# Performance work log

Hardware: AMD Instinct MI355X
Metric: run time of the kernel (lower is better)

Reference implementation:

```python
import jax, jax.numpy as jnp
import numpy as np

N_NODES = 50000
N_EDGES = 800000
F_IN = 128
HIDDEN = 128
N_CLASSES = 40


def setup_inputs() -> dict:
    key = jax.random.key(0)
    ks = jax.random.split(key, 8)
    x = jax.random.normal(ks[0], (N_NODES, F_IN), dtype=jnp.float32)
    edge_index = jax.random.randint(ks[1], (2, N_EDGES), 0, N_NODES, dtype=jnp.int32)
    s_in = 1.0 / np.sqrt(F_IN)
    s_h = 1.0 / np.sqrt(HIDDEN)
    W1_l = jax.random.normal(ks[2], (F_IN, HIDDEN), jnp.float32) * s_in
    W1_r = jax.random.normal(ks[3], (F_IN, HIDDEN), jnp.float32) * s_in
    b1 = jnp.zeros((HIDDEN,), jnp.float32)
    W2_l = jax.random.normal(ks[4], (HIDDEN, N_CLASSES), jnp.float32) * s_h
    W2_r = jax.random.normal(ks[5], (HIDDEN, N_CLASSES), jnp.float32) * s_h
    b2 = jnp.zeros((N_CLASSES,), jnp.float32)
    return {"x": x, "edge_index": edge_index, "W1_l": W1_l, "W1_r": W1_r,
            "b1": b1, "W2_l": W2_l, "W2_r": W2_r, "b2": b2}


def _sage_conv(x, src, dst, W_l, W_r, b):
    # mean-aggregate neighbor features at dst, then linear transform + root weight
    msg = x[src]                                                  # [E, d] gather
    agg = jax.ops.segment_sum(msg, dst, num_segments=N_NODES)     # [N, d] scatter-add
    deg = jax.ops.segment_sum(jnp.ones((src.shape[0],), x.dtype), dst,
                              num_segments=N_NODES)
    agg = agg / jnp.maximum(deg, 1.0)[:, None]                    # mean aggregation
    return agg @ W_l + x @ W_r + b


def reference(x, edge_index, W1_l, W1_r, b1, W2_l, W2_r, b2):
    src, dst = edge_index[0], edge_index[1]
    h = jax.nn.relu(_sage_conv(x, src, dst, W1_l, W1_r, b1))
    # F.dropout(p=0.5, training=self.training) -> identity in eval mode
    out = jax.nn.relu(_sage_conv(h, src, dst, W2_l, W2_r, b2))
    return jax.nn.log_softmax(out, axis=-1)
```

## Files before the change

kernel.cpp:

```cpp
#include <hip/hip_runtime.h>

#define N_NODES 50000
#define N_EDGES 800000
#define F_IN 128
#define HIDDEN 128
#define N_CLASSES 40

#define NBUCKET 391
#define BUCKET_CAP 4096
#define BINA_CHUNK 2048
#define BINA_NBLK 391
#define PREP_ITEMS (N_NODES * 32 + 128 * 256 + 80 * 128)
#define PREP_NBLK (PREP_ITEMS / 256)

#define OFF_RS     0
#define OFF_BCNT   50004
#define OFF_INVDEG 100004
#define OFF_SRCS   150004
#define OFF_AB     950004
#define OFF_BINS   7350004
#define OFF_PB     7350004
#define OFF_Q      8350004
#define OFF_WT1    10550004
#define OFF_WT2    10566388

typedef short bf16x8 __attribute__((ext_vector_type(8)));
typedef float f32x4 __attribute__((ext_vector_type(4)));
typedef unsigned short u16x8 __attribute__((ext_vector_type(8)));

static __device__ __forceinline__ unsigned short f2bf(float f) {
  unsigned int u = __builtin_bit_cast(unsigned int, f);
  u = (u + 0x7fffu + ((u >> 16) & 1u)) >> 16;
  return (unsigned short)u;
}
static __device__ __forceinline__ float bf2f(unsigned short s) {
  unsigned int u = ((unsigned int)s) << 16;
  return __builtin_bit_cast(float, u);
}

__global__ __launch_bounds__(256) void k_binA_prep(
    const int* __restrict__ src, const int* __restrict__ dst,
    int* __restrict__ bcnt, int* __restrict__ bins,
    const float* __restrict__ x, const float* __restrict__ W1l,
    const float* __restrict__ W1r, const float* __restrict__ W2l,
    const float* __restrict__ W2r, unsigned short* __restrict__ Ab,
    unsigned short* __restrict__ Wt1, unsigned short* __restrict__ Wt2) {
  if (blockIdx.x >= BINA_NBLK) {
    int idx = (blockIdx.x - BINA_NBLK) * 256 + threadIdx.x;
    if (idx < N_NODES * 32) {
      int row = idx >> 5, c4 = (idx & 31) << 2;
      const float4 v = *(const float4*)(x + (size_t)row * F_IN + c4);
      ushort4 o;
      o.x = f2bf(v.x); o.y = f2bf(v.y); o.z = f2bf(v.z); o.w = f2bf(v.w);
      *(ushort4*)(Ab + (size_t)row * 256 + 128 + c4) = o;
      return;
    }
    idx -= N_NODES * 32;
    if (idx < 128 * 256) {
      int n = idx >> 8, k = idx & 255;
      float v = (k < 128) ? W1l[(size_t)k * 128 + n]
                          : W1r[(size_t)(k - 128) * 128 + n];
      Wt1[(size_t)n * 256 + k] = f2bf(v);
    } else if (idx < 128 * 256 + 80 * 128) {
      int j = idx - 128 * 256;
      int n = j >> 7, k = j & 127;
      float v = (n < 40) ? W2l[(size_t)k * 40 + n]
                         : W2r[(size_t)k * 40 + (n - 40)];
      Wt2[(size_t)n * 128 + k] = f2bf(v);
    }
    return;
  }
  __shared__ int cnt[NBUCKET];
  __shared__ int excl[NBUCKET];
  __shared__ int cursor[NBUCKET];
  __shared__ int bbase[NBUCKET];
  __shared__ int sc[256];
  __shared__ int stage[BINA_CHUNK];
  __shared__ unsigned short bkt[BINA_CHUNK];
  int t = threadIdx.x;
  int e0 = blockIdx.x * BINA_CHUNK;
  int ne = N_EDGES - e0;
  if (ne > BINA_CHUNK) ne = BINA_CHUNK;
  for (int i = t; i < NBUCKET; i += 256) cnt[i] = 0;
  __syncthreads();
  for (int i = t; i < ne; i += 256) atomicAdd(&cnt[dst[e0 + i] >> 7], 1);
  __syncthreads();
  int a = (2 * t < NBUCKET) ? cnt[2 * t] : 0;
  int b2_ = (2 * t + 1 < NBUCKET) ? cnt[2 * t + 1] : 0;
  int s = a + b2_;
  sc[t] = s;
  __syncthreads();
  for (int off = 1; off < 256; off <<= 1) {
    int add = (t >= off) ? sc[t - off] : 0;
    __syncthreads();
    sc[t] += add;
    __syncthreads();
  }
  int pbase = sc[t] - s;
  if (2 * t < NBUCKET) { excl[2 * t] = pbase; cursor[2 * t] = pbase; }
  if (2 * t + 1 < NBUCKET) {
    excl[2 * t + 1] = pbase + a;
    cursor[2 * t + 1] = pbase + a;
  }
  for (int i = t; i < NBUCKET; i += 256)
    bbase[i] = atomicAdd(&bcnt[i], cnt[i]);
  __syncthreads();
  for (int i = t; i < ne; i += 256) {
    int d = dst[e0 + i];
    int sv = src[e0 + i];
    int b = d >> 7;
    int pos = atomicAdd(&cursor[b], 1);
    stage[pos] = ((d & 127) << 16) | sv;
    bkt[pos] = (unsigned short)b;
  }
  __syncthreads();
  for (int i = t; i < ne; i += 256) {
    int b = bkt[i];
    bins[(size_t)b * BUCKET_CAP + bbase[b] + (i - excl[b])] = stage[i];
  }
}

__global__ __launch_bounds__(256) void k_binB(
    const int* __restrict__ bcnt, const int* __restrict__ bins,
    int* __restrict__ rs, int* __restrict__ srcs,
    float* __restrict__ invdeg) {
  __shared__ int sc[256];
  __shared__ int hist[128];
  __shared__ int cursor[128];
  int b = blockIdx.x;
  int t = threadIdx.x;
  int v = 0;
  if (t < b) v += bcnt[t];
  if (t + 256 < b) v += bcnt[t + 256];
  sc[t] = v;
  __syncthreads();
  for (int off = 128; off; off >>= 1) {
    if (t < off) sc[t] += sc[t + off];
    __syncthreads();
  }
  int base = sc[0];
  int cnt = bcnt[b];
  const int* bb = bins + (size_t)b * BUCKET_CAP;
  if (t < 128) hist[t] = 0;
  __syncthreads();
  for (int i = t; i < cnt; i += 256) atomicAdd(&hist[bb[i] >> 16], 1);
  __syncthreads();
  int c = (t < 128) ? hist[t] : 0;
  sc[t] = c;
  __syncthreads();
  for (int off = 1; off < 128; off <<= 1) {
    int add = (t >= off) ? sc[t - off] : 0;
    __syncthreads();
    sc[t] += add;
    __syncthreads();
  }
  int lexcl = sc[t] - c;
  int node = b * 128 + t;
  if (t < 128 && node < N_NODES) {
    rs[node] = base + lexcl;
    invdeg[node] = 1.0f / (float)(c > 1 ? c : 1);
  }
  if (b == 0 && t == 0) rs[N_NODES] = N_EDGES;
  if (t < 128) cursor[t] = lexcl;
  __syncthreads();
  for (int i = t; i < cnt; i += 256) {
    int v2 = bb[i];
    int pos = atomicAdd(&cursor[v2 >> 16], 1);
    srcs[base + pos] = v2 & 0xFFFF;
  }
}

__global__ __launch_bounds__(256) void k_gather1(
    const int* __restrict__ rs, const int* __restrict__ srcs,
    const float* __restrict__ invdeg, unsigned short* __restrict__ Ab) {
  int node = blockIdx.x * 4 + (threadIdx.x >> 6);
  int lane = threadIdx.x & 63;
  int slot = lane >> 3, li = lane & 7;
  if (node >= N_NODES) return;
  int beg = rs[node], end = rs[node + 1];
  float acc[16];
#pragma unroll
  for (int j = 0; j < 16; j++) acc[j] = 0.f;
  for (int i = beg + slot; i < end; i += 8) {
    int s = srcs[i];
    const unsigned short* rp = Ab + (size_t)s * 256 + 128 + li * 8;
    u16x8 v0 = *(const u16x8*)rp;
    u16x8 v1 = *(const u16x8*)(rp + 64);
#pragma unroll
    for (int j = 0; j < 8; j++) {
      acc[j] += bf2f(v0[j]);
      acc[8 + j] += bf2f(v1[j]);
    }
  }
#pragma unroll
  for (int off = 8; off <= 32; off <<= 1)
#pragma unroll
    for (int j = 0; j < 16; j++) acc[j] += __shfl_xor(acc[j], off, 64);
  if (slot == 0) {
    float inv = invdeg[node];
    u16x8 o0, o1;
#pragma unroll
    for (int j = 0; j < 8; j++) {
      o0[j] = f2bf(acc[j] * inv);
      o1[j] = f2bf(acc[8 + j] * inv);
    }
    *(u16x8*)(Ab + (size_t)node * 256 + li * 8) = o0;
    *(u16x8*)(Ab + (size_t)node * 256 + 64 + li * 8) = o1;
  }
}

__global__ __launch_bounds__(256) void k_mlp(
    const unsigned short* __restrict__ Ab, const unsigned short* __restrict__ Wt1,
    const unsigned short* __restrict__ Wt2, const float* __restrict__ b1,
    const float* __restrict__ b2, unsigned short* __restrict__ pb,
    float* __restrict__ q) {
  __shared__ unsigned short hs[32 * 132];
  int w = threadIdx.x >> 6, lane = threadIdx.x & 63;
  int r = lane & 15, quad = lane >> 4;
  int row0 = blockIdx.x * 32;
  int ar0 = row0 + r;
  int ar1 = row0 + 16 + r;
  if (ar0 >= N_NODES) ar0 = N_NODES - 1;
  if (ar1 >= N_NODES) ar1 = N_NODES - 1;
  const unsigned short* Ap0 = Ab + (size_t)ar0 * 256 + quad * 8;
  const unsigned short* Ap1 = Ab + (size_t)ar1 * 256 + quad * 8;
  const unsigned short* Bp = Wt1 + (size_t)(w * 32 + r) * 256 + quad * 8;
  f32x4 acc[2][2];
#pragma unroll
  for (int nn = 0; nn < 2; nn++)
#pragma unroll
    for (int rt = 0; rt < 2; rt++) acc[nn][rt] = (f32x4){0.f, 0.f, 0.f, 0.f};
#pragma unroll
  for (int k0 = 0; k0 < 256; k0 += 32) {
    bf16x8 a0 = *(const bf16x8*)(Ap0 + k0);
    bf16x8 a1 = *(const bf16x8*)(Ap1 + k0);
#pragma unroll
    for (int nn = 0; nn < 2; nn++) {
      bf16x8 bv = *(const bf16x8*)(Bp + (size_t)nn * 16 * 256 + k0);
      acc[nn][0] = __builtin_amdgcn_mfma_f32_16x16x32_bf16(a0, bv, acc[nn][0], 0, 0, 0);
      acc[nn][1] = __builtin_amdgcn_mfma_f32_16x16x32_bf16(a1, bv, acc[nn][1], 0, 0, 0);
    }
  }
#pragma unroll
  for (int nn = 0; nn < 2; nn++) {
    int col = (w * 2 + nn) * 16 + r;
    float bias = b1[col];
#pragma unroll
    for (int rt = 0; rt < 2; rt++)
#pragma unroll
      for (int reg = 0; reg < 4; reg++)
        hs[(rt * 16 + quad * 4 + reg) * 132 + col] =
            f2bf(fmaxf(acc[nn][rt][reg] + bias, 0.f));
  }
  __syncthreads();
  int rt2 = w & 1, ng = w >> 1;
  int nbeg = ng ? 3 : 0;
  int ncnt = ng ? 2 : 3;
  const unsigned short* hrow = hs + (rt2 * 16 + r) * 132 + quad * 8;
  const unsigned short* Bp2 = Wt2 + (size_t)(nbeg * 16 + r) * 128 + quad * 8;
  f32x4 acc2[3];
#pragma unroll
  for (int j = 0; j < 3; j++) acc2[j] = (f32x4){0.f, 0.f, 0.f, 0.f};
#pragma unroll
  for (int k0 = 0; k0 < 128; k0 += 32) {
    ushort4 h0 = *(const ushort4*)(hrow + k0);
    ushort4 h1 = *(const ushort4*)(hrow + k0 + 4);
    bf16x8 af;
    af[0] = (short)h0.x; af[1] = (short)h0.y; af[2] = (short)h0.z; af[3] = (short)h0.w;
    af[4] = (short)h1.x; af[5] = (short)h1.y; af[6] = (short)h1.z; af[7] = (short)h1.w;
#pragma unroll
    for (int j = 0; j < 3; j++) {
      if (j < ncnt) {
        bf16x8 bv = *(const bf16x8*)(Bp2 + (size_t)j * 16 * 128 + k0);
        acc2[j] = __builtin_amdgcn_mfma_f32_16x16x32_bf16(af, bv, acc2[j], 0, 0, 0);
      }
    }
  }
  int crow0 = row0 + rt2 * 16 + quad * 4;
#pragma unroll
  for (int j = 0; j < 3; j++) {
    if (j < ncnt) {
      int col = (nbeg + j) * 16 + r;
#pragma unroll
      for (int reg = 0; reg < 4; reg++) {
        int row = crow0 + reg;
        if (row < N_NODES) {
          float v = acc2[j][reg];
          if (col < N_CLASSES)
            pb[(size_t)row * 40 + col] = f2bf(v);
          else
            q[(size_t)row * N_CLASSES + (col - N_CLASSES)] = v + b2[col - N_CLASSES];
        }
      }
    }
  }
}

__global__ __launch_bounds__(256) void k_final(
    const unsigned short* __restrict__ pb, const float* __restrict__ q,
    const int* __restrict__ rs, const int* __restrict__ srcs,
    const float* __restrict__ invdeg, float* __restrict__ out) {
  int node = blockIdx.x * 4 + (threadIdx.x >> 6);
  int lane = threadIdx.x & 63;
  int slot = lane >> 3, li = lane & 7;
  if (node >= N_NODES) return;
  bool valid = li < 5;
  int beg = rs[node], end = rs[node + 1];
  float acc[8];
#pragma unroll
  for (int j = 0; j < 8; j++) acc[j] = 0.f;
  for (int i = beg + slot; i < end; i += 8) {
    int s = srcs[i];
    if (valid) {
      u16x8 v = *(const u16x8*)(pb + (size_t)s * 40 + li * 8);
#pragma unroll
      for (int j = 0; j < 8; j++) acc[j] += bf2f(v[j]);
    }
  }
#pragma unroll
  for (int off = 8; off <= 32; off <<= 1)
#pragma unroll
    for (int j = 0; j < 8; j++) acc[j] += __shfl_xor(acc[j], off, 64);
  float inv = invdeg[node];
  float v[8];
  float m = -1e30f;
  if (valid) {
    const float* qr = q + (size_t)node * N_CLASSES + li * 8;
    float4 q0 = *(const float4*)qr;
    float4 q1 = *(const float4*)(qr + 4);
    v[0] = fmaxf(acc[0] * inv + q0.x, 0.f);
    v[1] = fmaxf(acc[1] * inv + q0.y, 0.f);
    v[2] = fmaxf(acc[2] * inv + q0.z, 0.f);
    v[3] = fmaxf(acc[3] * inv + q0.w, 0.f);
    v[4] = fmaxf(acc[4] * inv + q1.x, 0.f);
    v[5] = fmaxf(acc[5] * inv + q1.y, 0.f);
    v[6] = fmaxf(acc[6] * inv + q1.z, 0.f);
    v[7] = fmaxf(acc[7] * inv + q1.w, 0.f);
#pragma unroll
    for (int j = 0; j < 8; j++) m = fmaxf(m, v[j]);
  }
#pragma unroll
  for (int off = 1; off <= 4; off <<= 1) m = fmaxf(m, __shfl_xor(m, off, 8));
  float ssum = 0.f;
  if (valid) {
#pragma unroll
    for (int j = 0; j < 8; j++) ssum += __expf(v[j] - m);
  }
#pragma unroll
  for (int off = 1; off <= 4; off <<= 1) ssum += __shfl_xor(ssum, off, 8);
  float lse = __logf(ssum) + m;
  if (slot == 0 && valid) {
    float* orow = out + (size_t)node * N_CLASSES + li * 8;
    *(float4*)orow = make_float4(v[0] - lse, v[1] - lse, v[2] - lse, v[3] - lse);
    *(float4*)(orow + 4) =
        make_float4(v[4] - lse, v[5] - lse, v[6] - lse, v[7] - lse);
  }
}

extern "C" void kernel_launch(void* const* d_in, const int* in_sizes, int n_in,
                              void* d_out, int out_size, void* d_ws,
                              size_t ws_size, hipStream_t stream) {
  const float* x   = (const float*)d_in[0];
  const int*   ei  = (const int*)d_in[1];
  const int*   src = ei;
  const int*   dst = ei + N_EDGES;
  const float* W1l = (const float*)d_in[2];
  const float* W1r = (const float*)d_in[3];
  const float* b1  = (const float*)d_in[4];
  const float* W2l = (const float*)d_in[5];
  const float* W2r = (const float*)d_in[6];
  const float* b2  = (const float*)d_in[7];
  float* out = (float*)d_out;

  float* wsf = (float*)d_ws;
  int*   rs     = (int*)wsf + OFF_RS;
  int*   bcnt   = (int*)wsf + OFF_BCNT;
  float* invdeg = wsf + OFF_INVDEG;
  int*   srcs   = (int*)wsf + OFF_SRCS;
  unsigned short* Ab  = (unsigned short*)(wsf + OFF_AB);
  unsigned short* pb  = (unsigned short*)(wsf + OFF_PB);
  unsigned short* Wt1 = (unsigned short*)(wsf + OFF_WT1);
  unsigned short* Wt2 = (unsigned short*)(wsf + OFF_WT2);
  int*   bins   = (int*)wsf + OFF_BINS;
  float* q = wsf + OFF_Q;

  hipMemsetAsync(bcnt, 0, NBUCKET * sizeof(int), stream);

  k_binA_prep<<<BINA_NBLK + PREP_NBLK, 256, 0, stream>>>(
      src, dst, bcnt, bins, x, W1l, W1r, W2l, W2r, Ab, Wt1, Wt2);
  k_binB<<<NBUCKET, 256, 0, stream>>>(bcnt, bins, rs, srcs, invdeg);
  k_gather1<<<(N_NODES + 3) / 4, 256, 0, stream>>>(rs, srcs, invdeg, Ab);
  k_mlp<<<(N_NODES + 31) / 32, 256, 0, stream>>>(Ab, Wt1, Wt2, b1, b2, pb, q);
  k_final<<<(N_NODES + 3) / 4, 256, 0, stream>>>(pb, q, rs, srcs, invdeg, out);
}
```

Before: 223.2 us.

## Fuse layer-1 neighbor gather into MLP kernel via shared-memory A tile

Merges the separate gather kernel and the MLP kernel into one: each block gathers the mean-aggregated neighbor features for its 32 nodes directly into an LDS tile alongside the node's own bf16 features, then runs the MFMA GEMMs from LDS. This removes the global write and re-read of the aggregated activations and one kernel launch, and compacts the bf16 feature buffer to 128 columns. In exchange each wave now processes 8 nodes serially with fewer blocks in flight for the latency-bound gather, and LDS use per block grows, which may reduce occupancy.

```diff
diff --git a/kernel.cpp b/kernel.cpp
--- a/kernel.cpp
+++ b/kernel.cpp
@@ -17,7 +17,7 @@
 #define OFF_BCNT   50004
 #define OFF_INVDEG 100004
 #define OFF_SRCS   150004
-#define OFF_AB     950004
+#define OFF_XB     950004
 #define OFF_BINS   7350004
 #define OFF_PB     7350004
 #define OFF_Q      8350004
@@ -43,7 +43,7 @@
     int* __restrict__ bcnt, int* __restrict__ bins,
     const float* __restrict__ x, const float* __restrict__ W1l,
     const float* __restrict__ W1r, const float* __restrict__ W2l,
-    const float* __restrict__ W2r, unsigned short* __restrict__ Ab,
+    const float* __restrict__ W2r, unsigned short* __restrict__ xb,
     unsigned short* __restrict__ Wt1, unsigned short* __restrict__ Wt2) {
   if (blockIdx.x >= BINA_NBLK) {
     int idx = (blockIdx.x - BINA_NBLK) * 256 + threadIdx.x;
@@ -52,7 +52,7 @@
       const float4 v = *(const float4*)(x + (size_t)row * F_IN + c4);
       ushort4 o;
       o.x = f2bf(v.x); o.y = f2bf(v.y); o.z = f2bf(v.z); o.w = f2bf(v.w);
-      *(ushort4*)(Ab + (size_t)row * 256 + 128 + c4) = o;
+      *(ushort4*)(xb + (size_t)row * 128 + c4) = o;
       return;
     }
     idx -= N_NODES * 32;
@@ -170,77 +170,86 @@
   }
 }
 
-__global__ __launch_bounds__(256) void k_gather1(
-    const int* __restrict__ rs, const int* __restrict__ srcs,
-    const float* __restrict__ invdeg, unsigned short* __restrict__ Ab) {
-  int node = blockIdx.x * 4 + (threadIdx.x >> 6);
-  int lane = threadIdx.x & 63;
-  int slot = lane >> 3, li = lane & 7;
-  if (node >= N_NODES) return;
-  int beg = rs[node], end = rs[node + 1];
-  float acc[16];
-#pragma unroll
-  for (int j = 0; j < 16; j++) acc[j] = 0.f;
-  for (int i = beg + slot; i < end; i += 8) {
-    int s = srcs[i];
-    const unsigned short* rp = Ab + (size_t)s * 256 + 128 + li * 8;
-    u16x8 v0 = *(const u16x8*)rp;
-    u16x8 v1 = *(const u16x8*)(rp + 64);
-#pragma unroll
-    for (int j = 0; j < 8; j++) {
-      acc[j] += bf2f(v0[j]);
-      acc[8 + j] += bf2f(v1[j]);
-    }
-  }
-#pragma unroll
-  for (int off = 8; off <= 32; off <<= 1)
-#pragma unroll
-    for (int j = 0; j < 16; j++) acc[j] += __shfl_xor(acc[j], off, 64);
-  if (slot == 0) {
-    float inv = invdeg[node];
-    u16x8 o0, o1;
-#pragma unroll
-    for (int j = 0; j < 8; j++) {
-      o0[j] = f2bf(acc[j] * inv);
-      o1[j] = f2bf(acc[8 + j] * inv);
-    }
-    *(u16x8*)(Ab + (size_t)node * 256 + li * 8) = o0;
-    *(u16x8*)(Ab + (size_t)node * 256 + 64 + li * 8) = o1;
-  }
-}
-
-__global__ __launch_bounds__(256) void k_mlp(
-    const unsigned short* __restrict__ Ab, const unsigned short* __restrict__ Wt1,
-    const unsigned short* __restrict__ Wt2, const float* __restrict__ b1,
-    const float* __restrict__ b2, unsigned short* __restrict__ pb,
-    float* __restrict__ q) {
+__global__ __launch_bounds__(256) void k_fused(
+    const unsigned short* __restrict__ xb, const int* __restrict__ rs,
+    const int* __restrict__ srcs, const float* __restrict__ invdeg,
+    const unsigned short* __restrict__ Wt1, const unsigned short* __restrict__ Wt2,
+    const float* __restrict__ b1, const float* __restrict__ b2,
+    unsigned short* __restrict__ pb, float* __restrict__ q) {
+  __shared__ unsigned short as[32 * 264];
   __shared__ unsigned short hs[32 * 132];
   int w = threadIdx.x >> 6, lane = threadIdx.x & 63;
+  int t = threadIdx.x;
+  int row0 = blockIdx.x * 32;
+
+  for (int chunk = t; chunk < 32 * 16; chunk += 256) {
+    int lrow = chunk >> 4, c8 = (chunk & 15) * 8;
+    int grow = row0 + lrow;
+    if (grow >= N_NODES) grow = N_NODES - 1;
+    u16x8 v = *(const u16x8*)(xb + (size_t)grow * 128 + c8);
+    *(u16x8*)(as + lrow * 264 + 128 + c8) = v;
+  }
+
+  int slot = lane >> 3, li = lane & 7;
+  for (int j = 0; j < 8; j++) {
+    int lrow = w * 8 + j;
+    int node = row0 + lrow;
+    int beg = 0, end = 0;
+    if (node < N_NODES) { beg = rs[node]; end = rs[node + 1]; }
+    float acc[16];
+#pragma unroll
+    for (int k = 0; k < 16; k++) acc[k] = 0.f;
+    for (int i = beg + slot; i < end; i += 8) {
+      int s = srcs[i];
+      const unsigned short* rp = xb + (size_t)s * 128 + li * 8;
+      u16x8 v0 = *(const u16x8*)rp;
+      u16x8 v1 = *(const u16x8*)(rp + 64);
+#pragma unroll
+      for (int k = 0; k < 8; k++) {
+        acc[k] += bf2f(v0[k]);
+        acc[8 + k] += bf2f(v1[k]);
+      }
+    }
+#pragma unroll
+    for (int off = 8; off <= 32; off <<= 1)
+#pragma unroll
+      for (int k = 0; k < 16; k++) acc[k] += __shfl_xor(acc[k], off, 64);
+    if (slot == 0) {
+      int nidx = (node < N_NODES) ? node : 0;
+      float inv = invdeg[nidx];
+      u16x8 o0, o1;
+#pragma unroll
+      for (int k = 0; k < 8; k++) {
+        o0[k] = f2bf(acc[k] * inv);
+        o1[k] = f2bf(acc[8 + k] * inv);
+      }
+      *(u16x8*)(as + lrow * 264 + li * 8) = o0;
+      *(u16x8*)(as + lrow * 264 + 64 + li * 8) = o1;
+    }
+  }
+  __syncthreads();
+
   int r = lane & 15, quad = lane >> 4;
-  int row0 = blockIdx.x * 32;
-  int ar0 = row0 + r;
-  int ar1 = row0 + 16 + r;
-  if (ar0 >= N_NODES) ar0 = N_NODES - 1;
-  if (ar1 >= N_NODES) ar1 = N_NODES - 1;
-  const unsigned short* Ap0 = Ab + (size_t)ar0 * 256 + quad * 8;
-  const unsigned short* Ap1 = Ab + (size_t)ar1 * 256 + quad * 8;
   const unsigned short* Bp = Wt1 + (size_t)(w * 32 + r) * 256 + quad * 8;
-  f32x4 acc[2][2];
+  const unsigned short* A0 = as + r * 264 + quad * 8;
+  const unsigned short* A1 = as + (16 + r) * 264 + quad * 8;
+  f32x4 acc1[2][2];
 #pragma unroll
   for (int nn = 0; nn < 2; nn++)
 #pragma unroll
-    for (int rt = 0; rt < 2; rt++) acc[nn][rt] = (f32x4){0.f, 0.f, 0.f, 0.f};
+    for (int rt = 0; rt < 2; rt++) acc1[nn][rt] = (f32x4){0.f, 0.f, 0.f, 0.f};
 #pragma unroll
   for (int k0 = 0; k0 < 256; k0 += 32) {
-    bf16x8 a0 = *(const bf16x8*)(Ap0 + k0);
-    bf16x8 a1 = *(const bf16x8*)(Ap1 + k0);
+    bf16x8 a0 = *(const bf16x8*)(A0 + k0);
+    bf16x8 a1 = *(const bf16x8*)(A1 + k0);
 #pragma unroll
     for (int nn = 0; nn < 2; nn++) {
       bf16x8 bv = *(const bf16x8*)(Bp + (size_t)nn * 16 * 256 + k0);
-      acc[nn][0] = __builtin_amdgcn_mfma_f32_16x16x32_bf16(a0, bv, acc[nn][0], 0, 0, 0);
-      acc[nn][1] = __builtin_amdgcn_mfma_f32_16x16x32_bf16(a1, bv, acc[nn][1], 0, 0, 0);
-    }
-  }
+      acc1[nn][0] = __builtin_amdgcn_mfma_f32_16x16x32_bf16(a0, bv, acc1[nn][0], 0, 0, 0);
+      acc1[nn][1] = __builtin_amdgcn_mfma_f32_16x16x32_bf16(a1, bv, acc1[nn][1], 0, 0, 0);
+    }
+  }
+  __syncthreads();
 #pragma unroll
   for (int nn = 0; nn < 2; nn++) {
     int col = (w * 2 + nn) * 16 + r;
@@ -250,9 +259,10 @@
 #pragma unroll
       for (int reg = 0; reg < 4; reg++)
         hs[(rt * 16 + quad * 4 + reg) * 132 + col] =
-            f2bf(fmaxf(acc[nn][rt][reg] + bias, 0.f));
-  }
-  __syncthreads();
+            f2bf(fmaxf(acc1[nn][rt][reg] + bias, 0.f));
+  }
+  __syncthreads();
+
   int rt2 = w & 1, ng = w >> 1;
   int nbeg = ng ? 3 : 0;
   int ncnt = ng ? 2 : 3;
@@ -377,7 +387,7 @@
   int*   bcnt   = (int*)wsf + OFF_BCNT;
   float* invdeg = wsf + OFF_INVDEG;
   int*   srcs   = (int*)wsf + OFF_SRCS;
-  unsigned short* Ab  = (unsigned short*)(wsf + OFF_AB);
+  unsigned short* xb  = (unsigned short*)(wsf + OFF_XB);
   unsigned short* pb  = (unsigned short*)(wsf + OFF_PB);
   unsigned short* Wt1 = (unsigned short*)(wsf + OFF_WT1);
   unsigned short* Wt2 = (unsigned short*)(wsf + OFF_WT2);
@@ -387,9 +397,9 @@
   hipMemsetAsync(bcnt, 0, NBUCKET * sizeof(int), stream);
 
   k_binA_prep<<<BINA_NBLK + PREP_NBLK, 256, 0, stream>>>(
-      src, dst, bcnt, bins, x, W1l, W1r, W2l, W2r, Ab, Wt1, Wt2);
+      src, dst, bcnt, bins, x, W1l, W1r, W2l, W2r, xb, Wt1, Wt2);
   k_binB<<<NBUCKET, 256, 0, stream>>>(bcnt, bins, rs, srcs, invdeg);
-  k_gather1<<<(N_NODES + 3) / 4, 256, 0, stream>>>(rs, srcs, invdeg, Ab);
-  k_mlp<<<(N_NODES + 31) / 32, 256, 0, stream>>>(Ab, Wt1, Wt2, b1, b2, pb, q);
+  k_fused<<<(N_NODES + 31) / 32, 256, 0, stream>>>(
+      xb, rs, srcs, invdeg, Wt1, Wt2, b1, b2, pb, q);
   k_final<<<(N_NODES + 3) / 4, 256, 0, stream>>>(pb, q, rs, srcs, invdeg, out);
 }
```

Result: faster. 212.7 us (-4.7%).
